# Optimization experiments

Measured on AMD Instinct MI355X. Metric: run time of the kernel, lower is better.

The kernel has to match this reference:

```python
import jax, jax.numpy as jnp
import numpy as np

B, V, E, N = 4, 16384, 4, 32
F, U = 1024, 1024


def setup_inputs() -> dict:
    key = jax.random.key(0)
    k1, k2, k3 = jax.random.split(key, 3)
    # adjacency values in [-1, V); -1 marks non-existent neighbours
    adjacency = jax.random.randint(k1, (B, V, E, N), -1, V, dtype=jnp.int32)
    # force some vertices to be fully invalid (all -1) so the mask path matters
    invalid_vertex = jax.random.uniform(k2, (B, V, 1, 1)) < 0.25
    adjacency = jnp.where(invalid_vertex, jnp.int32(-1), adjacency)
    features = jax.random.normal(k3, (B, V, F), dtype=jnp.float32)
    kernel = jax.random.normal(jax.random.fold_in(key, 10), (F, U), dtype=jnp.float32) * (1.0 / np.sqrt(F))
    bias = jnp.zeros((U,), dtype=jnp.float32)
    return {"adjacency": adjacency, "features": features, "kernel": kernel, "bias": bias}


def reference(adjacency, features, kernel, bias):
    # A vertex is "valid" if it has at least one neighbour (any adjacency entry >= 0)
    valid = jnp.any(adjacency >= 0, axis=(2, 3))  # [B, V]
    # Dense per-node linear transform (1x1-conv analogue) + bias + relu
    out = jax.nn.relu(jnp.einsum('bvf,fu->bvu', features, kernel) + bias)  # [B, V, U]
    f_in, f_out = kernel.shape
    if f_in == f_out:
        def_features = features  # invalid vertices keep their input features
    else:
        def_features = jnp.zeros(features.shape[:-1] + (f_out,), dtype=features.dtype)
    # scatter transformed features back only at valid vertices
    return jnp.where(valid[..., None], out, def_features)
```

## Files before the change

kernel.cpp:

```cpp
#include <hip/hip_runtime.h>

#define MTOT 65536
#define KTOT 1024
#define NTOT 1024

#define BM 256
#define BN 256
#define BK 64
#define NTILE (KTOT / BK)

typedef __attribute__((ext_vector_type(4))) unsigned int u32x4;
typedef __attribute__((ext_vector_type(4))) float f32x4;
typedef __attribute__((ext_vector_type(8))) __bf16 bf16x8;
typedef __attribute__((ext_vector_type(4))) unsigned short u16x4;

static __device__ __forceinline__ unsigned short f2bf(float f) {
    unsigned int u = __float_as_uint(f);
    u += 0x7fffu + ((u >> 16) & 1u);
    return (unsigned short)(u >> 16);
}

#define GLOAD16(g, l)                                                              \
    __builtin_amdgcn_global_load_lds(                                              \
        (const __attribute__((address_space(1))) void*)(g),                        \
        (__attribute__((address_space(3))) void*)(l), 16, 0, 0)

#define VMCNT(n) asm volatile("s_waitcnt vmcnt(" #n ")" ::: "memory")
#define LGKM0    asm volatile("s_waitcnt lgkmcnt(0)" ::: "memory")
#define CFENCE   asm volatile("" ::: "memory")
#define SBAR     __builtin_amdgcn_sched_barrier(0)
#define BAR()    __builtin_amdgcn_s_barrier()

__global__ __launch_bounds__(256) void prep_kernel(const int* __restrict__ adj,
                                                   const float* __restrict__ feat,
                                                   unsigned short* __restrict__ abf,
                                                   unsigned char* __restrict__ valid,
                                                   float* __restrict__ out) {
    const int row  = blockIdx.x * 4 + (threadIdx.x >> 6);
    const int lane = threadIdx.x & 63;
    const int2 a2  = reinterpret_cast<const int2*>(adj)[(size_t)row * 64 + lane];
    const bool anyv = __any((a2.x >= 0) || (a2.y >= 0)) != 0;

    const f32x4* frow = reinterpret_cast<const f32x4*>(feat + (size_t)row * KTOT);
    u16x4*       brow = reinterpret_cast<u16x4*>(abf + (size_t)row * KTOT);
    f32x4*       orow = reinterpret_cast<f32x4*>(out + (size_t)row * NTOT);
    if (anyv) {
#pragma unroll
        for (int i = 0; i < 4; ++i) {
            const f32x4 v = frow[lane + 64 * i];
            u16x4 b;
            b.x = f2bf(v[0]); b.y = f2bf(v[1]); b.z = f2bf(v[2]); b.w = f2bf(v[3]);
            brow[lane + 64 * i] = b;
        }
    } else {
#pragma unroll
        for (int i = 0; i < 4; ++i)
            orow[lane + 64 * i] = frow[lane + 64 * i];
    }
    if (lane == 0) valid[row] = anyv ? 1 : 0;
}

__global__ __launch_bounds__(256) void transposeB_kernel(const float* __restrict__ kern,
                                                         unsigned short* __restrict__ kT) {
    __shared__ float tile[32][33];
    const int bx = blockIdx.x & 31;
    const int by = blockIdx.x >> 5;
    const int tx = threadIdx.x & 31;
    const int ty = threadIdx.x >> 5;
#pragma unroll
    for (int r = 0; r < 4; ++r)
        tile[ty + r * 8][tx] = kern[(size_t)(by * 32 + ty + r * 8) * NTOT + bx * 32 + tx];
    __syncthreads();
#pragma unroll
    for (int r = 0; r < 4; ++r)
        kT[(size_t)(bx * 32 + ty + r * 8) * KTOT + by * 32 + tx] = f2bf(tile[tx][ty + r * 8]);
}

__global__ __launch_bounds__(512, 2) void gemm_kernel(const unsigned short* __restrict__ A,
                                                      const unsigned short* __restrict__ Bt,
                                                      const float* __restrict__ bias,
                                                      const unsigned char* __restrict__ valid,
                                                      float* __restrict__ out) {
    __shared__ __align__(16) unsigned short Asm[32768];
    __shared__ __align__(16) unsigned short Bsm[32768];

    const int tid  = threadIdx.x;
    const int lane = tid & 63;
    const int wv   = tid >> 6;
    const int wm   = wv >> 2;
    const int wn   = wv & 3;

    const int cpx = (int)gridDim.x >> 3;
    const int swz = ((int)blockIdx.x & 7) * cpx + ((int)blockIdx.x >> 3);
    const int bm  = swz >> 2;
    const int bn  = swz & 3;
    const size_t m0 = (size_t)bm * BM;
    const int    n0 = bn * BN;

    const int s_goff = (wv * 8 + (lane >> 3)) * KTOT + (((lane & 7) ^ ((lane >> 3) & 7)) << 3);
    const int s_loff = wv << 9;

    const unsigned short* Agl = A  + m0 * (size_t)KTOT;
    const unsigned short* Bgl = Bt + (size_t)n0 * KTOT;

#define STAGE_A(d, h, kt) do {                                                      \
        const unsigned short* _s = Agl + (size_t)((h) * 128) * KTOT + (kt) * 64 + s_goff; \
        unsigned short* _l = &Asm[(d) * 16384 + (h) * 8192 + s_loff];               \
        GLOAD16(_s, _l);                                                            \
        GLOAD16(_s + (size_t)64 * KTOT, _l + 4096);                                 \
    } while (0)
#define STAGE_B(d, h, kt) do {                                                      \
        const unsigned short* _s = Bgl + (size_t)((h) * 128) * KTOT + (kt) * 64 + s_goff; \
        unsigned short* _l = &Bsm[(d) * 16384 + (h) * 8192 + s_loff];               \
        GLOAD16(_s, _l);                                                            \
        GLOAD16(_s + (size_t)64 * KTOT, _l + 4096);                                 \
    } while (0)

    const int lr = lane & 15;
    const int g4 = lane >> 4;
    const int chunk = (g4 ^ (lr & 7)) << 3;
    const int abase = wm * 8192 + lr * 64 + chunk;
    const int bbase = (wn >> 1) * 8192 + (wn & 1) * 4096 + lr * 64 + chunk;

#define AFR(d, m, kh) __builtin_bit_cast(bf16x8, \
        *reinterpret_cast<const u32x4*>(&Asm[(d) * 16384 + (m) * 1024 + (abase ^ ((kh) * 32))]))
#define BFR(d, n, kh) __builtin_bit_cast(bf16x8, \
        *reinterpret_cast<const u32x4*>(&Bsm[(d) * 16384 + (n) * 1024 + (bbase ^ ((kh) * 32))]))

#define RDA(d, mb) do {                                                             \
        aX[0][0] = AFR(d, (mb), 0);     aX[0][1] = AFR(d, (mb), 1);                 \
        aX[1][0] = AFR(d, (mb) + 1, 0); aX[1][1] = AFR(d, (mb) + 1, 1);             \
    } while (0)
#define RDB(d) do {                                                                 \
        _Pragma("unroll") for (int _n = 0; _n < 4; ++_n) {                          \
            Bc[_n][0] = BFR(d, _n, 0); Bc[_n][1] = BFR(d, _n, 1); }                 \
    } while (0)

    f32x4 acc[8][4];
#pragma unroll
    for (int m = 0; m < 8; ++m)
#pragma unroll
        for (int n = 0; n < 4; ++n)
            acc[m][n] = {0.0f, 0.0f, 0.0f, 0.0f};

#define MFMA_PH(M0) do {                                                            \
        __builtin_amdgcn_s_setprio(1);                                              \
        _Pragma("unroll") for (int _kh = 0; _kh < 2; ++_kh)                         \
        _Pragma("unroll") for (int _i = 0; _i < 2; ++_i)                            \
        _Pragma("unroll") for (int _n = 0; _n < 4; ++_n)                            \
            acc[(M0) + _i][_n] = __builtin_amdgcn_mfma_f32_16x16x32_bf16(           \
                aX[_i][_kh], Bc[_n][_kh], acc[(M0) + _i][_n], 0, 0, 0);             \
        __builtin_amdgcn_s_setprio(0);                                              \
    } while (0)

    bf16x8 aX[2][2], Bc[4][2];

    STAGE_A(0, 0, 0); STAGE_A(0, 1, 0); STAGE_B(0, 0, 0); STAGE_B(0, 1, 0);
    STAGE_B(1, 0, 1); STAGE_B(1, 1, 1);
    VMCNT(4);
    BAR(); CFENCE;

    for (int i = 0; i < NTILE / 2; ++i) {
        const int t1 = 2 * i + 1, t2 = 2 * i + 2, t3 = 2 * i + 3;
        const bool s2 = t2 < NTILE, s3 = t3 < NTILE;

        RDB(0); RDA(0, 0);
        STAGE_A(1, 0, t1);
        BAR(); CFENCE; LGKM0; SBAR;
        MFMA_PH(0);
        BAR(); CFENCE;
        RDA(0, 2);
        STAGE_A(1, 1, t1);
        BAR(); CFENCE; LGKM0; SBAR;
        MFMA_PH(2);
        BAR(); CFENCE;
        RDA(0, 4);
        if (s2) STAGE_B(0, 0, t2);
        BAR(); CFENCE; LGKM0; SBAR;
        MFMA_PH(4);
        BAR(); CFENCE;
        RDA(0, 6);
        if (s2) STAGE_B(0, 1, t2);
        BAR(); CFENCE; LGKM0; SBAR;
        MFMA_PH(6);
        if (s2) VMCNT(4); else VMCNT(0);
        BAR(); CFENCE;
        RDB(1); RDA(1, 0);
        if (s2) STAGE_A(0, 0, t2);
        BAR(); CFENCE; LGKM0; SBAR;
        MFMA_PH(0);
        BAR(); CFENCE;
        RDA(1, 2);
        if (s2) STAGE_A(0, 1, t2);
        BAR(); CFENCE; LGKM0; SBAR;
        MFMA_PH(2);
        BAR(); CFENCE;
        RDA(1, 4);
        if (s3) STAGE_B(1, 0, t3);
        BAR(); CFENCE; LGKM0; SBAR;
        MFMA_PH(4);
        BAR(); CFENCE;
        RDA(1, 6);
        if (s3) STAGE_B(1, 1, t3);
        BAR(); CFENCE; LGKM0; SBAR;
        MFMA_PH(6);
        if (s3) { VMCNT(4); }
        else if (s2) { VMCNT(0); }
        BAR(); CFENCE;
    }

    float bv[4];
#pragma unroll
    for (int n = 0; n < 4; ++n)
        bv[n] = bias[n0 + wn * 64 + n * 16 + lr];

#pragma unroll
    for (int m = 0; m < 8; ++m) {
#pragma unroll
        for (int q = 0; q < 4; ++q) {
            const size_t row = m0 + wm * 128 + m * 16 + g4 * 4 + q;
            if (valid[row]) {
                const size_t ro = row * NTOT + n0 + wn * 64 + lr;
#pragma unroll
                for (int n = 0; n < 4; ++n)
                    out[ro + n * 16] = fmaxf(acc[m][n][q] + bv[n], 0.0f);
            }
        }
    }
#undef STAGE_A
#undef STAGE_B
#undef AFR
#undef BFR
#undef RDA
#undef RDB
#undef MFMA_PH
}

#define FBM 128
#define FBN 128
#define FBK 32

__global__ __launch_bounds__(256) void valid_kernel(const int* __restrict__ adj,
                                                    unsigned char* __restrict__ valid) {
    const int row  = blockIdx.x * 4 + (threadIdx.x >> 6);
    const int lane = threadIdx.x & 63;
    const int2 v = reinterpret_cast<const int2*>(adj)[(size_t)row * 64 + lane];
    const int anyv = __any((v.x >= 0) || (v.y >= 0));
    if (lane == 0) valid[row] = anyv ? 1 : 0;
}

__global__ __launch_bounds__(256) void gemm_fb(const float* __restrict__ A,
                                               const unsigned short* __restrict__ Bt,
                                               const float* __restrict__ bias,
                                               const unsigned char* __restrict__ valid,
                                               float* __restrict__ out) {
    __shared__ __align__(16) unsigned short Asm[2][FBM * FBK];
    __shared__ __align__(16) unsigned short Bsm[2][FBN * FBK];
    const int tid = threadIdx.x;
    const int bm = blockIdx.x >> 3;
    const int bn = blockIdx.x & 7;
    const size_t m0 = (size_t)bm * FBM;
    const int n0 = bn * FBN;
    const int ja = tid & 7, ra0 = tid >> 3;
    const int jb = tid & 3, rb0 = tid >> 2;
    const int wv = tid >> 6, wr = wv >> 1, wc = wv & 1;
    const int lane = tid & 63, lr = lane & 15, g = lane >> 4;
    f32x4 acc[4][4];
#pragma unroll
    for (int m = 0; m < 4; ++m)
#pragma unroll
        for (int n = 0; n < 4; ++n) acc[m][n] = {0.f, 0.f, 0.f, 0.f};
    int awidx[4], bwidx[2], aridx[4], bridx[4];
#pragma unroll
    for (int t = 0; t < 4; ++t) {
        const int row = ra0 + t * 32;
        awidx[t] = row * 32 + (((ja >> 1) ^ ((row >> 1) & 3)) * 8) + (ja & 1) * 4;
    }
#pragma unroll
    for (int t = 0; t < 2; ++t) {
        const int row = rb0 + t * 64;
        bwidx[t] = row * 32 + ((jb ^ ((row >> 1) & 3)) * 8);
    }
#pragma unroll
    for (int m = 0; m < 4; ++m) {
        const int row = wr * 64 + m * 16 + lr;
        aridx[m] = row * 32 + ((g ^ ((row >> 1) & 3)) * 8);
    }
#pragma unroll
    for (int n = 0; n < 4; ++n) {
        const int row = wc * 64 + n * 16 + lr;
        bridx[n] = row * 32 + ((g ^ ((row >> 1) & 3)) * 8);
    }
    const int NT = KTOT / FBK;
    f32x4 areg[4];
    u32x4 breg[2];
#pragma unroll
    for (int t = 0; t < 4; ++t)
        areg[t] = reinterpret_cast<const f32x4*>(A + (m0 + ra0 + t * 32) * KTOT)[ja];
#pragma unroll
    for (int t = 0; t < 2; ++t)
        breg[t] = reinterpret_cast<const u32x4*>(Bt + (size_t)(n0 + rb0 + t * 64) * KTOT)[jb];
#pragma unroll
    for (int t = 0; t < 4; ++t) {
        unsigned long long w = (unsigned long long)f2bf(areg[t][0]) |
                               ((unsigned long long)f2bf(areg[t][1]) << 16) |
                               ((unsigned long long)f2bf(areg[t][2]) << 32) |
                               ((unsigned long long)f2bf(areg[t][3]) << 48);
        *reinterpret_cast<unsigned long long*>(&Asm[0][awidx[t]]) = w;
    }
#pragma unroll
    for (int t = 0; t < 2; ++t) *reinterpret_cast<u32x4*>(&Bsm[0][bwidx[t]]) = breg[t];
    int cur = 0;
    for (int kt = 0; kt < NT; ++kt) {
        const bool more = (kt + 1) < NT;
        if (more) {
            const int koff = (kt + 1) * FBK;
#pragma unroll
            for (int t = 0; t < 4; ++t)
                areg[t] = reinterpret_cast<const f32x4*>(A + (m0 + ra0 + t * 32) * KTOT + koff)[ja];
#pragma unroll
            for (int t = 0; t < 2; ++t)
                breg[t] = reinterpret_cast<const u32x4*>(Bt + (size_t)(n0 + rb0 + t * 64) * KTOT + koff)[jb];
        }
        __syncthreads();
        bf16x8 af[4], bfr[4];
#pragma unroll
        for (int m = 0; m < 4; ++m)
            af[m] = __builtin_bit_cast(bf16x8, *reinterpret_cast<const u32x4*>(&Asm[cur][aridx[m]]));
#pragma unroll
        for (int n = 0; n < 4; ++n)
            bfr[n] = __builtin_bit_cast(bf16x8, *reinterpret_cast<const u32x4*>(&Bsm[cur][bridx[n]]));
#pragma unroll
        for (int m = 0; m < 4; ++m)
#pragma unroll
            for (int n = 0; n < 4; ++n)
                acc[m][n] = __builtin_amdgcn_mfma_f32_16x16x32_bf16(af[m], bfr[n], acc[m][n], 0, 0, 0);
        if (more) {
            const int nxt = cur ^ 1;
#pragma unroll
            for (int t = 0; t < 4; ++t) {
                unsigned long long w = (unsigned long long)f2bf(areg[t][0]) |
                                       ((unsigned long long)f2bf(areg[t][1]) << 16) |
                                       ((unsigned long long)f2bf(areg[t][2]) << 32) |
                                       ((unsigned long long)f2bf(areg[t][3]) << 48);
                *reinterpret_cast<unsigned long long*>(&Asm[nxt][awidx[t]]) = w;
            }
#pragma unroll
            for (int t = 0; t < 2; ++t) *reinterpret_cast<u32x4*>(&Bsm[nxt][bwidx[t]]) = breg[t];
        }
        cur ^= 1;
    }
    float bv[4];
#pragma unroll
    for (int n = 0; n < 4; ++n) bv[n] = bias[n0 + wc * 64 + n * 16 + lr];
#pragma unroll
    for (int m = 0; m < 4; ++m) {
#pragma unroll
        for (int q = 0; q < 4; ++q) {
            const size_t row = m0 + wr * 64 + m * 16 + g * 4 + q;
            const bool v = valid[row] != 0;
            const size_t ro = row * (size_t)NTOT;
#pragma unroll
            for (int n = 0; n < 4; ++n) {
                const int col = n0 + wc * 64 + n * 16 + lr;
                out[ro + col] = v ? fmaxf(acc[m][n][q] + bv[n], 0.0f) : A[ro + col];
            }
        }
    }
}

extern "C" void kernel_launch(void* const* d_in, const int* in_sizes, int n_in,
                              void* d_out, int out_size, void* d_ws, size_t ws_size,
                              hipStream_t stream) {
    const int*   adj  = (const int*)d_in[0];
    const float* feat = (const float*)d_in[1];
    const float* kern = (const float*)d_in[2];
    const float* bias = (const float*)d_in[3];
    float* out = (float*)d_out;

    unsigned short* kT    = (unsigned short*)d_ws;
    unsigned char*  valid = (unsigned char*)d_ws + 2 * 1024 * 1024;
    unsigned short* abf   = (unsigned short*)((char*)d_ws + 2 * 1024 * 1024 + 65536);

    const size_t need = 2ull * 1024 * 1024 + 65536 + (size_t)MTOT * KTOT * 2;

    transposeB_kernel<<<(KTOT / 32) * (NTOT / 32), 256, 0, stream>>>(kern, kT);
    if (ws_size >= need) {
        prep_kernel<<<MTOT / 4, 256, 0, stream>>>(adj, feat, abf, valid, out);
        gemm_kernel<<<(MTOT / BM) * (NTOT / BN), 512, 0, stream>>>(abf, kT, bias, valid, out);
    } else {
        valid_kernel<<<MTOT / 4, 256, 0, stream>>>(adj, valid);
        gemm_fb<<<(MTOT / FBM) * (NTOT / FBN), 256, 0, stream>>>(feat, kT, bias, valid, out);
    }
}
```

Measured before the change: 259.4 us.

## Fuse fp32-to-bf16 conversion of features into GEMM A-tile loading

Removes the prep pass that wrote a bf16 copy of the features. The GEMM now loads fp32 A through registers, converts it to bf16, and stores the swizzled result into LDS, with the pipeline waits reworked around this. Invalid rows copy the input features in the epilogue, and the workspace-size fallback GEMM is dropped. The aim is to save the extra bf16 write/read traffic and a kernel launch. In exchange, A is read in fp32 by each N-tile block, with higher register use and synchronous loads instead of direct-to-LDS loads.

```diff
diff --git a/kernel.cpp b/kernel.cpp
--- a/kernel.cpp
+++ b/kernel.cpp
@@ -12,13 +12,6 @@
 typedef __attribute__((ext_vector_type(4))) unsigned int u32x4;
 typedef __attribute__((ext_vector_type(4))) float f32x4;
 typedef __attribute__((ext_vector_type(8))) __bf16 bf16x8;
-typedef __attribute__((ext_vector_type(4))) unsigned short u16x4;
-
-static __device__ __forceinline__ unsigned short f2bf(float f) {
-    unsigned int u = __float_as_uint(f);
-    u += 0x7fffu + ((u >> 16) & 1u);
-    return (unsigned short)(u >> 16);
-}
 
 #define GLOAD16(g, l)                                                              \
     __builtin_amdgcn_global_load_lds(                                              \
@@ -31,32 +24,25 @@
 #define SBAR     __builtin_amdgcn_sched_barrier(0)
 #define BAR()    __builtin_amdgcn_s_barrier()
 
-__global__ __launch_bounds__(256) void prep_kernel(const int* __restrict__ adj,
-                                                   const float* __restrict__ feat,
-                                                   unsigned short* __restrict__ abf,
-                                                   unsigned char* __restrict__ valid,
-                                                   float* __restrict__ out) {
+static __device__ __forceinline__ unsigned short f2bf(float f) {
+    unsigned int u = __float_as_uint(f);
+    u += 0x7fffu + ((u >> 16) & 1u);
+    return (unsigned short)(u >> 16);
+}
+
+static __device__ __forceinline__ bf16x8 cvt8(f32x4 a, f32x4 b) {
+    bf16x8 r;
+    r[0] = (__bf16)a[0]; r[1] = (__bf16)a[1]; r[2] = (__bf16)a[2]; r[3] = (__bf16)a[3];
+    r[4] = (__bf16)b[0]; r[5] = (__bf16)b[1]; r[6] = (__bf16)b[2]; r[7] = (__bf16)b[3];
+    return r;
+}
+
+__global__ __launch_bounds__(256) void valid_kernel(const int* __restrict__ adj,
+                                                    unsigned char* __restrict__ valid) {
     const int row  = blockIdx.x * 4 + (threadIdx.x >> 6);
     const int lane = threadIdx.x & 63;
-    const int2 a2  = reinterpret_cast<const int2*>(adj)[(size_t)row * 64 + lane];
-    const bool anyv = __any((a2.x >= 0) || (a2.y >= 0)) != 0;
-
-    const f32x4* frow = reinterpret_cast<const f32x4*>(feat + (size_t)row * KTOT);
-    u16x4*       brow = reinterpret_cast<u16x4*>(abf + (size_t)row * KTOT);
-    f32x4*       orow = reinterpret_cast<f32x4*>(out + (size_t)row * NTOT);
-    if (anyv) {
-#pragma unroll
-        for (int i = 0; i < 4; ++i) {
-            const f32x4 v = frow[lane + 64 * i];
-            u16x4 b;
-            b.x = f2bf(v[0]); b.y = f2bf(v[1]); b.z = f2bf(v[2]); b.w = f2bf(v[3]);
-            brow[lane + 64 * i] = b;
-        }
-    } else {
-#pragma unroll
-        for (int i = 0; i < 4; ++i)
-            orow[lane + 64 * i] = frow[lane + 64 * i];
-    }
+    const int2 v = reinterpret_cast<const int2*>(adj)[(size_t)row * 64 + lane];
+    const int anyv = __any((v.x >= 0) || (v.y >= 0));
     if (lane == 0) valid[row] = anyv ? 1 : 0;
 }
 
@@ -76,7 +62,7 @@
         kT[(size_t)(bx * 32 + ty + r * 8) * KTOT + by * 32 + tx] = f2bf(tile[tx][ty + r * 8]);
 }
 
-__global__ __launch_bounds__(512, 2) void gemm_kernel(const unsigned short* __restrict__ A,
+__global__ __launch_bounds__(512, 2) void gemm_kernel(const float* __restrict__ A,
                                                       const unsigned short* __restrict__ Bt,
                                                       const float* __restrict__ bias,
                                                       const unsigned char* __restrict__ valid,
@@ -99,21 +85,30 @@
 
     const int s_goff = (wv * 8 + (lane >> 3)) * KTOT + (((lane & 7) ^ ((lane >> 3) & 7)) << 3);
     const int s_loff = wv << 9;
-
-    const unsigned short* Agl = A  + m0 * (size_t)KTOT;
     const unsigned short* Bgl = Bt + (size_t)n0 * KTOT;
 
-#define STAGE_A(d, h, kt) do {                                                      \
-        const unsigned short* _s = Agl + (size_t)((h) * 128) * KTOT + (kt) * 64 + s_goff; \
-        unsigned short* _l = &Asm[(d) * 16384 + (h) * 8192 + s_loff];               \
-        GLOAD16(_s, _l);                                                            \
-        GLOAD16(_s + (size_t)64 * KTOT, _l + 4096);                                 \
-    } while (0)
 #define STAGE_B(d, h, kt) do {                                                      \
         const unsigned short* _s = Bgl + (size_t)((h) * 128) * KTOT + (kt) * 64 + s_goff; \
         unsigned short* _l = &Bsm[(d) * 16384 + (h) * 8192 + s_loff];               \
         GLOAD16(_s, _l);                                                            \
         GLOAD16(_s + (size_t)64 * KTOT, _l + 4096);                                 \
+    } while (0)
+
+    const int arow = wv * 8 + (lane >> 3);
+    const int ac   = lane & 7;
+    const float* Agl = A + (m0 + arow) * (size_t)KTOT + ac * 8;
+    const int awb = arow * 64 + (((ac) ^ (arow & 7)) * 8);
+
+#define ALOAD(dst, h, kt) do {                                                      \
+        const float* _p = Agl + (size_t)((h) * 128) * KTOT + (kt) * 64;             \
+        dst[0] = *reinterpret_cast<const f32x4*>(_p);                               \
+        dst[1] = *reinterpret_cast<const f32x4*>(_p + 4);                           \
+        dst[2] = *reinterpret_cast<const f32x4*>(_p + (size_t)64 * KTOT);           \
+        dst[3] = *reinterpret_cast<const f32x4*>(_p + (size_t)64 * KTOT + 4);       \
+    } while (0)
+#define AWRITE(d, h, src) do {                                                      \
+        *reinterpret_cast<bf16x8*>(&Asm[(d) * 16384 + (h) * 8192 + awb])        = cvt8(src[0], src[1]); \
+        *reinterpret_cast<bf16x8*>(&Asm[(d) * 16384 + (h) * 8192 + awb + 4096]) = cvt8(src[2], src[3]); \
     } while (0)
 
     const int lr = lane & 15;
@@ -154,58 +149,62 @@
     } while (0)
 
     bf16x8 aX[2][2], Bc[4][2];
-
-    STAGE_A(0, 0, 0); STAGE_A(0, 1, 0); STAGE_B(0, 0, 0); STAGE_B(0, 1, 0);
+    f32x4 as0[4], as1[4];
+
+    ALOAD(as0, 0, 0); ALOAD(as1, 1, 0);
+    STAGE_B(0, 0, 0); STAGE_B(0, 1, 0);
     STAGE_B(1, 0, 1); STAGE_B(1, 1, 1);
+    VMCNT(8);
+    AWRITE(0, 0, as0); AWRITE(0, 1, as1);
     VMCNT(4);
-    BAR(); CFENCE;
-
+    LGKM0; BAR(); CFENCE;
+
+#pragma unroll 1
     for (int i = 0; i < NTILE / 2; ++i) {
         const int t1 = 2 * i + 1, t2 = 2 * i + 2, t3 = 2 * i + 3;
-        const bool s2 = t2 < NTILE, s3 = t3 < NTILE;
+        const bool full = (i < NTILE / 2 - 1);
 
         RDB(0); RDA(0, 0);
-        STAGE_A(1, 0, t1);
+        ALOAD(as0, 0, t1);
         BAR(); CFENCE; LGKM0; SBAR;
         MFMA_PH(0);
         BAR(); CFENCE;
         RDA(0, 2);
-        STAGE_A(1, 1, t1);
+        ALOAD(as1, 1, t1);
         BAR(); CFENCE; LGKM0; SBAR;
         MFMA_PH(2);
         BAR(); CFENCE;
         RDA(0, 4);
-        if (s2) STAGE_B(0, 0, t2);
+        if (full) { STAGE_B(0, 0, t2); VMCNT(6); } else { VMCNT(4); }
+        AWRITE(1, 0, as0);
         BAR(); CFENCE; LGKM0; SBAR;
         MFMA_PH(4);
         BAR(); CFENCE;
         RDA(0, 6);
-        if (s2) STAGE_B(0, 1, t2);
+        if (full) { STAGE_B(0, 1, t2); VMCNT(4); } else { VMCNT(0); }
+        AWRITE(1, 1, as1);
         BAR(); CFENCE; LGKM0; SBAR;
         MFMA_PH(6);
-        if (s2) VMCNT(4); else VMCNT(0);
         BAR(); CFENCE;
         RDB(1); RDA(1, 0);
-        if (s2) STAGE_A(0, 0, t2);
+        if (full) ALOAD(as0, 0, t2);
         BAR(); CFENCE; LGKM0; SBAR;
         MFMA_PH(0);
         BAR(); CFENCE;
         RDA(1, 2);
-        if (s2) STAGE_A(0, 1, t2);
+        if (full) ALOAD(as1, 1, t2);
         BAR(); CFENCE; LGKM0; SBAR;
         MFMA_PH(2);
         BAR(); CFENCE;
         RDA(1, 4);
-        if (s3) STAGE_B(1, 0, t3);
+        if (full) { STAGE_B(1, 0, t3); VMCNT(6); AWRITE(0, 0, as0); }
         BAR(); CFENCE; LGKM0; SBAR;
         MFMA_PH(4);
         BAR(); CFENCE;
         RDA(1, 6);
-        if (s3) STAGE_B(1, 1, t3);
+        if (full) { STAGE_B(1, 1, t3); VMCNT(4); AWRITE(0, 1, as1); }
         BAR(); CFENCE; LGKM0; SBAR;
         MFMA_PH(6);
-        if (s3) { VMCNT(4); }
-        else if (s2) { VMCNT(0); }
         BAR(); CFENCE;
     }
 
@@ -219,154 +218,26 @@
 #pragma unroll
         for (int q = 0; q < 4; ++q) {
             const size_t row = m0 + wm * 128 + m * 16 + g4 * 4 + q;
+            const size_t ro  = row * NTOT + n0 + wn * 64 + lr;
             if (valid[row]) {
-                const size_t ro = row * NTOT + n0 + wn * 64 + lr;
 #pragma unroll
                 for (int n = 0; n < 4; ++n)
                     out[ro + n * 16] = fmaxf(acc[m][n][q] + bv[n], 0.0f);
+            } else {
+#pragma unroll
+                for (int n = 0; n < 4; ++n)
+                    out[ro + n * 16] = A[ro + n * 16];
             }
         }
     }
-#undef STAGE_A
 #undef STAGE_B
+#undef ALOAD
+#undef AWRITE
 #undef AFR
 #undef BFR
 #undef RDA
 #undef RDB
 #undef MFMA_PH
-}
-
-#define FBM 128
-#define FBN 128
-#define FBK 32
-
-__global__ __launch_bounds__(256) void valid_kernel(const int* __restrict__ adj,
-                                                    unsigned char* __restrict__ valid) {
-    const int row  = blockIdx.x * 4 + (threadIdx.x >> 6);
-    const int lane = threadIdx.x & 63;
-    const int2 v = reinterpret_cast<const int2*>(adj)[(size_t)row * 64 + lane];
-    const int anyv = __any((v.x >= 0) || (v.y >= 0));
-    if (lane == 0) valid[row] = anyv ? 1 : 0;
-}
-
-__global__ __launch_bounds__(256) void gemm_fb(const float* __restrict__ A,
-                                               const unsigned short* __restrict__ Bt,
-                                               const float* __restrict__ bias,
-                                               const unsigned char* __restrict__ valid,
-                                               float* __restrict__ out) {
-    __shared__ __align__(16) unsigned short Asm[2][FBM * FBK];
-    __shared__ __align__(16) unsigned short Bsm[2][FBN * FBK];
-    const int tid = threadIdx.x;
-    const int bm = blockIdx.x >> 3;
-    const int bn = blockIdx.x & 7;
-    const size_t m0 = (size_t)bm * FBM;
-    const int n0 = bn * FBN;
-    const int ja = tid & 7, ra0 = tid >> 3;
-    const int jb = tid & 3, rb0 = tid >> 2;
-    const int wv = tid >> 6, wr = wv >> 1, wc = wv & 1;
-    const int lane = tid & 63, lr = lane & 15, g = lane >> 4;
-    f32x4 acc[4][4];
-#pragma unroll
-    for (int m = 0; m < 4; ++m)
-#pragma unroll
-        for (int n = 0; n < 4; ++n) acc[m][n] = {0.f, 0.f, 0.f, 0.f};
-    int awidx[4], bwidx[2], aridx[4], bridx[4];
-#pragma unroll
-    for (int t = 0; t < 4; ++t) {
-        const int row = ra0 + t * 32;
-        awidx[t] = row * 32 + (((ja >> 1) ^ ((row >> 1) & 3)) * 8) + (ja & 1) * 4;
-    }
-#pragma unroll
-    for (int t = 0; t < 2; ++t) {
-        const int row = rb0 + t * 64;
-        bwidx[t] = row * 32 + ((jb ^ ((row >> 1) & 3)) * 8);
-    }
-#pragma unroll
-    for (int m = 0; m < 4; ++m) {
-        const int row = wr * 64 + m * 16 + lr;
-        aridx[m] = row * 32 + ((g ^ ((row >> 1) & 3)) * 8);
-    }
-#pragma unroll
-    for (int n = 0; n < 4; ++n) {
-        const int row = wc * 64 + n * 16 + lr;
-        bridx[n] = row * 32 + ((g ^ ((row >> 1) & 3)) * 8);
-    }
-    const int NT = KTOT / FBK;
-    f32x4 areg[4];
-    u32x4 breg[2];
-#pragma unroll
-    for (int t = 0; t < 4; ++t)
-        areg[t] = reinterpret_cast<const f32x4*>(A + (m0 + ra0 + t * 32) * KTOT)[ja];
-#pragma unroll
-    for (int t = 0; t < 2; ++t)
-        breg[t] = reinterpret_cast<const u32x4*>(Bt + (size_t)(n0 + rb0 + t * 64) * KTOT)[jb];
-#pragma unroll
-    for (int t = 0; t < 4; ++t) {
-        unsigned long long w = (unsigned long long)f2bf(areg[t][0]) |
-                               ((unsigned long long)f2bf(areg[t][1]) << 16) |
-                               ((unsigned long long)f2bf(areg[t][2]) << 32) |
-                               ((unsigned long long)f2bf(areg[t][3]) << 48);
-        *reinterpret_cast<unsigned long long*>(&Asm[0][awidx[t]]) = w;
-    }
-#pragma unroll
-    for (int t = 0; t < 2; ++t) *reinterpret_cast<u32x4*>(&Bsm[0][bwidx[t]]) = breg[t];
-    int cur = 0;
-    for (int kt = 0; kt < NT; ++kt) {
-        const bool more = (kt + 1) < NT;
-        if (more) {
-            const int koff = (kt + 1) * FBK;
-#pragma unroll
-            for (int t = 0; t < 4; ++t)
-                areg[t] = reinterpret_cast<const f32x4*>(A + (m0 + ra0 + t * 32) * KTOT + koff)[ja];
-#pragma unroll
-            for (int t = 0; t < 2; ++t)
-                breg[t] = reinterpret_cast<const u32x4*>(Bt + (size_t)(n0 + rb0 + t * 64) * KTOT + koff)[jb];
-        }
-        __syncthreads();
-        bf16x8 af[4], bfr[4];
-#pragma unroll
-        for (int m = 0; m < 4; ++m)
-            af[m] = __builtin_bit_cast(bf16x8, *reinterpret_cast<const u32x4*>(&Asm[cur][aridx[m]]));
-#pragma unroll
-        for (int n = 0; n < 4; ++n)
-            bfr[n] = __builtin_bit_cast(bf16x8, *reinterpret_cast<const u32x4*>(&Bsm[cur][bridx[n]]));
-#pragma unroll
-        for (int m = 0; m < 4; ++m)
-#pragma unroll
-            for (int n = 0; n < 4; ++n)
-                acc[m][n] = __builtin_amdgcn_mfma_f32_16x16x32_bf16(af[m], bfr[n], acc[m][n], 0, 0, 0);
-        if (more) {
-            const int nxt = cur ^ 1;
-#pragma unroll
-            for (int t = 0; t < 4; ++t) {
-                unsigned long long w = (unsigned long long)f2bf(areg[t][0]) |
-                                       ((unsigned long long)f2bf(areg[t][1]) << 16) |
-                                       ((unsigned long long)f2bf(areg[t][2]) << 32) |
-                                       ((unsigned long long)f2bf(areg[t][3]) << 48);
-                *reinterpret_cast<unsigned long long*>(&Asm[nxt][awidx[t]]) = w;
-            }
-#pragma unroll
-            for (int t = 0; t < 2; ++t) *reinterpret_cast<u32x4*>(&Bsm[nxt][bwidx[t]]) = breg[t];
-        }
-        cur ^= 1;
-    }
-    float bv[4];
-#pragma unroll
-    for (int n = 0; n < 4; ++n) bv[n] = bias[n0 + wc * 64 + n * 16 + lr];
-#pragma unroll
-    for (int m = 0; m < 4; ++m) {
-#pragma unroll
-        for (int q = 0; q < 4; ++q) {
-            const size_t row = m0 + wr * 64 + m * 16 + g * 4 + q;
-            const bool v = valid[row] != 0;
-            const size_t ro = row * (size_t)NTOT;
-#pragma unroll
-            for (int n = 0; n < 4; ++n) {
-                const int col = n0 + wc * 64 + n * 16 + lr;
-                out[ro + col] = v ? fmaxf(acc[m][n][q] + bv[n], 0.0f) : A[ro + col];
-            }
-        }
-    }
 }
 
 extern "C" void kernel_launch(void* const* d_in, const int* in_sizes, int n_in,
@@ -380,16 +251,8 @@
 
     unsigned short* kT    = (unsigned short*)d_ws;
     unsigned char*  valid = (unsigned char*)d_ws + 2 * 1024 * 1024;
-    unsigned short* abf   = (unsigned short*)((char*)d_ws + 2 * 1024 * 1024 + 65536);
-
-    const size_t need = 2ull * 1024 * 1024 + 65536 + (size_t)MTOT * KTOT * 2;
 
     transposeB_kernel<<<(KTOT / 32) * (NTOT / 32), 256, 0, stream>>>(kern, kT);
-    if (ws_size >= need) {
-        prep_kernel<<<MTOT / 4, 256, 0, stream>>>(adj, feat, abf, valid, out);
-        gemm_kernel<<<(MTOT / BM) * (NTOT / BN), 512, 0, stream>>>(abf, kT, bias, valid, out);
-    } else {
-        valid_kernel<<<MTOT / 4, 256, 0, stream>>>(adj, valid);
-        gemm_fb<<<(MTOT / FBM) * (NTOT / FBN), 256, 0, stream>>>(feat, kT, bias, valid, out);
-    }
-}
+    valid_kernel<<<MTOT / 4, 256, 0, stream>>>(adj, valid);
+    gemm_kernel<<<(MTOT / BM) * (NTOT / BN), 512, 0, stream>>>(feat, kT, bias, valid, out);
+}
```

Result: slower. 288.6 us (+11.2%).
